# Kernel tuning notes

Hardware: AMD Instinct MI355X
Metric: run time of the kernel (lower is better)

Reference implementation:

```python
import jax, jax.numpy as jnp
import numpy as np

D_MODEL = 512
STATE_DIM = 64
INNER = 768  # ceil(512 * 1.5)
KERNEL = 3
EPS = 1e-5
DELTA_MIN = 1e-4
DELTA_MAX = 3.0


def _hippo_legS(n):
    A = np.zeros((n, n), dtype=np.float32)
    for i in range(n):
        ci = np.sqrt(2 * i + 1)
        for m in range(i + 1):
            cm = np.sqrt(2 * m + 1)
            if i == m:
                A[i, m] = -(2 * i + 1)
            else:
                sign = -1.0 if (i - m) % 2 == 0 else 1.0
                A[i, m] = sign * ci * cm
    idx = np.arange(n, dtype=np.float32)
    B = np.sqrt(2.0 * idx + 1.0)
    C = B.copy()
    C[1::2] *= -1.0
    return A, B, C


def setup_inputs() -> dict:
    key = jax.random.key(0)
    k1, k2, k3, k4 = jax.random.split(key, 4)
    x = jax.random.normal(k1, (8, 2048, D_MODEL), dtype=jnp.float32)
    norm_w = jnp.ones((D_MODEL,), jnp.float32)
    norm_b = jnp.zeros((D_MODEL,), jnp.float32)
    W_in = jax.random.normal(k2, (D_MODEL, 3 * INNER), jnp.float32) * 0.02
    conv_w = jax.random.normal(k3, (INNER, KERNEL), jnp.float32) * 0.2  # torch (C,1,k) squeezed
    A_np, B_np, C_np = _hippo_legS(STATE_DIM)
    scale = 1.0 / np.sqrt(INNER)
    A = jnp.asarray(A_np)
    B_mat = jnp.asarray(np.repeat(B_np[:, None], INNER, axis=1) * scale)   # [N, inner]
    C_mat = jnp.asarray(np.repeat(C_np[None, :], INNER, axis=0) * scale)   # [inner, N]
    W_out = jax.random.normal(k4, (INNER, D_MODEL), jnp.float32) * 0.02
    return {"x": x, "norm_w": norm_w, "norm_b": norm_b, "W_in": W_in,
            "conv_w": conv_w, "A": A, "B_mat": B_mat, "C_mat": C_mat, "W_out": W_out}


def reference(x, norm_w, norm_b, W_in, conv_w, A, B_mat, C_mat, W_out):
    Bsz, L, D = x.shape
    N = A.shape[0]
    # LayerNorm (biased variance, as torch)
    mu = x.mean(-1, keepdims=True)
    var = jnp.mean((x - mu) ** 2, axis=-1, keepdims=True)
    h = (x - mu) / jnp.sqrt(var + EPS) * norm_w + norm_b
    proj = h @ W_in                                 # [B, L, 3*inner]
    data, gate, delta_raw = jnp.split(proj, 3, axis=-1)
    # causal depthwise conv: torch pads k-1 both sides then truncates to L
    k = conv_w.shape[1]
    xp = jnp.pad(data, ((0, 0), (k - 1, 0), (0, 0)))
    kern = conv_w.T[:, None, :]                     # [k, 1, inner] (WIO)
    conv = jax.lax.conv_general_dilated(
        xp, kern, window_strides=(1,), padding='VALID',
        dimension_numbers=('NWC', 'WIO', 'NWC'), feature_group_count=INNER)
    u = jax.nn.silu(conv)                           # [B, L, inner]
    delta = jnp.minimum(jax.nn.softplus(delta_raw).mean(-1) + DELTA_MIN, DELTA_MAX)  # [B, L]
    I = jnp.eye(N, dtype=x.dtype)

    def step(state, inp):
        u_t, dt = inp                               # [B, inner], [B]
        Bu = jnp.einsum('nd,bd->bn', B_mat, u_t)    # [B, N]
        rhs = state + dt[:, None] * Bu
        mat = I - dt[:, None, None] * A             # [B, N, N]
        st = jnp.linalg.solve(mat, rhs[..., None])[..., 0]
        y = jnp.einsum('dn,bn->bd', C_mat, st)      # [B, inner]
        return st, y

    state0 = jnp.zeros((Bsz, N), x.dtype)
    _, ys = jax.lax.scan(step, state0, (jnp.swapaxes(u, 0, 1), delta.T))
    selective = jnp.swapaxes(ys, 0, 1)              # [B, L, inner]
    gated = jax.nn.sigmoid(gate) * selective
    return x + gated @ W_out
```

## Files before the change

### kernel.cpp

```cpp
#include <hip/hip_runtime.h>

typedef unsigned short u16;
typedef short short8 __attribute__((ext_vector_type(8)));
typedef float f32x4 __attribute__((ext_vector_type(4)));

#define D_MODEL 512
#define INNER 768
#define N3 2304
#define LSEQ 2048
#define BATCH 8
#define MROWS 16384

constexpr size_t OFF_H     = 0;
constexpr size_t OFF_WINT  = 16777216;
constexpr size_t OFF_WOUTT = 19136512;
constexpr size_t OFF_DATA  = 19922944;
constexpr size_t OFF_GATE  = 45088768;
constexpr size_t OFF_DSUM  = 70254592;
constexpr size_t OFF_YBAR  = 70451200;
constexpr size_t WS_NEEDED = 70516736;

__device__ __forceinline__ u16 f2bf(float f) {
  unsigned u = __builtin_bit_cast(unsigned, f);
  u += 0x7fffu + ((u >> 16) & 1u);
  return (u16)(u >> 16);
}
__device__ __forceinline__ float bf2f(u16 h) {
  unsigned u = ((unsigned)h) << 16;
  return __builtin_bit_cast(float, u);
}

__device__ __forceinline__ float dpp_shr1(float x) {
  int r = __builtin_amdgcn_update_dpp(0, __builtin_bit_cast(int, x),
                                      0x138 , 0xf, 0xf, true);
  return __builtin_bit_cast(float, r);
}

#if __has_builtin(__builtin_amdgcn_global_load_lds)
#define HAVE_GLLDS 1
__device__ __forceinline__ void gl_lds16(const u16* g, u16* l) {
  __builtin_amdgcn_global_load_lds(
      (const __attribute__((address_space(1))) unsigned int*)g,
      (__attribute__((address_space(3))) unsigned int*)l, 16, 0, 0);
}
#else
#define HAVE_GLLDS 0
#endif

__global__ __launch_bounds__(256) void transp_cast(const float* __restrict__ in,
                                                   u16* __restrict__ out, int R, int C) {
  __shared__ float tile[32][33];
  int c0 = blockIdx.x * 32, r0 = blockIdx.y * 32;
  int tx = threadIdx.x, ty = threadIdx.y;
#pragma unroll
  for (int i = 0; i < 4; ++i)
    tile[ty + i * 8][tx] = in[(size_t)(r0 + ty + i * 8) * C + c0 + tx];
  __syncthreads();
#pragma unroll
  for (int i = 0; i < 4; ++i)
    out[(size_t)(c0 + ty + i * 8) * R + r0 + tx] = f2bf(tile[tx][ty + i * 8]);
}

__global__ __launch_bounds__(256) void ln_kernel(const float* __restrict__ x,
                                                 const float* __restrict__ gw,
                                                 const float* __restrict__ gb,
                                                 u16* __restrict__ h) {
  int row = blockIdx.x * 4 + (threadIdx.x >> 6);
  int lane = threadIdx.x & 63;
  const float* xr = x + (size_t)row * D_MODEL;
  float4 v0 = *(const float4*)(xr + lane * 4);
  float4 v1 = *(const float4*)(xr + 256 + lane * 4);
  float s  = v0.x + v0.y + v0.z + v0.w + v1.x + v1.y + v1.z + v1.w;
  float s2 = v0.x * v0.x + v0.y * v0.y + v0.z * v0.z + v0.w * v0.w +
             v1.x * v1.x + v1.y * v1.y + v1.z * v1.z + v1.w * v1.w;
#pragma unroll
  for (int m = 1; m < 64; m <<= 1) { s += __shfl_xor(s, m); s2 += __shfl_xor(s2, m); }
  float mu = s * (1.0f / 512.0f);
  float var = s2 * (1.0f / 512.0f) - mu * mu;
  float rstd = rsqrtf(var + 1e-5f);
  float4 w0 = *(const float4*)(gw + lane * 4);
  float4 w1 = *(const float4*)(gw + 256 + lane * 4);
  float4 b0 = *(const float4*)(gb + lane * 4);
  float4 b1 = *(const float4*)(gb + 256 + lane * 4);
  float y0 = (v0.x - mu) * rstd * w0.x + b0.x;
  float y1 = (v0.y - mu) * rstd * w0.y + b0.y;
  float y2 = (v0.z - mu) * rstd * w0.z + b0.z;
  float y3 = (v0.w - mu) * rstd * w0.w + b0.w;
  float y4 = (v1.x - mu) * rstd * w1.x + b1.x;
  float y5 = (v1.y - mu) * rstd * w1.y + b1.y;
  float y6 = (v1.z - mu) * rstd * w1.z + b1.z;
  float y7 = (v1.w - mu) * rstd * w1.w + b1.w;
  uint2 pa, pb;
  pa.x = (unsigned)f2bf(y0) | ((unsigned)f2bf(y1) << 16);
  pa.y = (unsigned)f2bf(y2) | ((unsigned)f2bf(y3) << 16);
  pb.x = (unsigned)f2bf(y4) | ((unsigned)f2bf(y5) << 16);
  pb.y = (unsigned)f2bf(y6) | ((unsigned)f2bf(y7) << 16);
  *(uint2*)(h + (size_t)row * D_MODEL + lane * 4) = pa;
  *(uint2*)(h + (size_t)row * D_MODEL + 256 + lane * 4) = pb;
}

template <int MODE>
__global__ __launch_bounds__(256) void gemm_bt(
    const u16* __restrict__ A, const u16* __restrict__ BT, int M, int N, int K,
    u16* __restrict__ dataBuf, u16* __restrict__ gateSig, float* __restrict__ deltaSum,
    const float* __restrict__ ybarp, const float* __restrict__ xres,
    float* __restrict__ outp) {
  __shared__ u16 As[128 * 32];
  __shared__ u16 Bs[128 * 32];
  int tid = threadIdx.x;
  int lane = tid & 63, wv = tid >> 6;
  int wm = wv >> 1, wn = wv & 1;
  int m0 = blockIdx.y * 128, n0 = blockIdx.x * 128;
  f32x4 acc[4][4];
#pragma unroll
  for (int i = 0; i < 4; ++i)
#pragma unroll
    for (int j = 0; j < 4; ++j) acc[i][j] = (f32x4)0.0f;

  int r4 = tid >> 2;
  int c4 = (tid & 3) * 8;
  int nsteps = K >> 5;
  int mrow = wm * 64 + (lane & 15);
  int nrow = wn * 64 + (lane & 15);
  int kq = (lane >> 4) * 8;

  const u16* Ab = A + (size_t)(m0 + r4) * K + c4;
  const u16* Bb = BT + (size_t)(n0 + r4) * K + c4;
  const size_t rowA = (size_t)64 * K, rowB = (size_t)64 * K;
  u16* lA0 = &As[tid * 8];
  u16* lA1 = &As[(tid + 256) * 8];
  u16* lB0 = &Bs[tid * 8];
  u16* lB1 = &Bs[(tid + 256) * 8];

  for (int step = 0; step < nsteps; ++step) {
    int k0 = step * 32;
    __syncthreads();
#if HAVE_GLLDS
    gl_lds16(Ab + k0, lA0);
    gl_lds16(Ab + k0 + rowA, lA1);
    gl_lds16(Bb + k0, lB0);
    gl_lds16(Bb + k0 + rowB, lB1);
#else
    uint4 a0 = *(const uint4*)(Ab + k0);
    uint4 a1 = *(const uint4*)(Ab + k0 + rowA);
    uint4 b0 = *(const uint4*)(Bb + k0);
    uint4 b1 = *(const uint4*)(Bb + k0 + rowB);
    *(uint4*)lA0 = a0; *(uint4*)lA1 = a1;
    *(uint4*)lB0 = b0; *(uint4*)lB1 = b1;
#endif
    __syncthreads();
    short8 af[4], bfr[4];
#pragma unroll
    for (int mt = 0; mt < 4; ++mt)
      af[mt] = *(const short8*)(&As[(mrow + mt * 16) * 32 + kq]);
#pragma unroll
    for (int nt = 0; nt < 4; ++nt)
      bfr[nt] = *(const short8*)(&Bs[(nrow + nt * 16) * 32 + kq]);
#pragma unroll
    for (int mt = 0; mt < 4; ++mt)
#pragma unroll
      for (int nt = 0; nt < 4; ++nt)
        acc[mt][nt] = __builtin_amdgcn_mfma_f32_16x16x32_bf16(af[mt], bfr[nt], acc[mt][nt], 0, 0, 0);
  }

  if (MODE == 1) {
    int region = (n0 >= 1536) ? 2 : (n0 >= 768 ? 1 : 0);
    if (region < 2) {
      u16* dst = (region == 0) ? dataBuf : gateSig;
#pragma unroll
      for (int mt = 0; mt < 4; ++mt) {
        int rbase = m0 + wm * 64 + mt * 16 + (lane >> 4) * 4;
#pragma unroll
        for (int nt = 0; nt < 4; ++nt) {
          int col = n0 - region * 768 + wn * 64 + nt * 16 + (lane & 15);
#pragma unroll
          for (int r = 0; r < 4; ++r) {
            float val = acc[mt][nt][r];
            if (region == 1) val = 1.0f / (1.0f + __expf(-val));
            dst[(size_t)(rbase + r) * INNER + col] = f2bf(val);
          }
        }
      }
    } else {
#pragma unroll
      for (int mt = 0; mt < 4; ++mt) {
        int rbase = m0 + wm * 64 + mt * 16 + (lane >> 4) * 4;
        float sums[4] = {0.f, 0.f, 0.f, 0.f};
#pragma unroll
        for (int nt = 0; nt < 4; ++nt)
#pragma unroll
          for (int r = 0; r < 4; ++r) {
            float xv = acc[mt][nt][r];
            sums[r] += fmaxf(xv, 0.0f) + __logf(1.0f + __expf(-fabsf(xv)));
          }
#pragma unroll
        for (int r = 0; r < 4; ++r) {
          float val = sums[r];
          val += __shfl_xor(val, 1); val += __shfl_xor(val, 2);
          val += __shfl_xor(val, 4); val += __shfl_xor(val, 8);
          if ((lane & 15) == 0) atomicAdd(&deltaSum[rbase + r], val);
        }
      }
    }
  } else {
#pragma unroll
    for (int mt = 0; mt < 4; ++mt) {
      int rbase = m0 + wm * 64 + mt * 16 + (lane >> 4) * 4;
#pragma unroll
      for (int r = 0; r < 4; ++r) {
        float yr = ybarp[rbase + r] * 0.036084391824351615f;
#pragma unroll
        for (int nt = 0; nt < 4; ++nt) {
          int col = n0 + wn * 64 + nt * 16 + (lane & 15);
          size_t o = (size_t)(rbase + r) * D_MODEL + col;
          outp[o] = xres[o] + yr * acc[mt][nt][r];
        }
      }
    }
  }
}

__global__ __launch_bounds__(256) void conv_reduce(const u16* __restrict__ dataBuf,
                                                   const float* __restrict__ conv_w,
                                                   const float* __restrict__ deltaSum,
                                                   float2* __restrict__ pairsG) {
  int r = blockIdx.x;
  int b = r >> 11;
  int t = r & (LSEQ - 1);
  int tid = threadIdx.x;
  float part = 0.0f;
#pragma unroll
  for (int j = 0; j < 3; ++j) {
    int d = tid + j * 256;
    float cw0 = conv_w[d * 3 + 0], cw1 = conv_w[d * 3 + 1], cw2 = conv_w[d * 3 + 2];
    float x2 = bf2f(dataBuf[(size_t)r * INNER + d]);
    float x1 = (t >= 1) ? bf2f(dataBuf[(size_t)(r - 1) * INNER + d]) : 0.0f;
    float x0 = (t >= 2) ? bf2f(dataBuf[(size_t)(r - 2) * INNER + d]) : 0.0f;
    float c = cw0 * x0 + cw1 * x1 + cw2 * x2;
    part += c / (1.0f + __expf(-c));
  }
#pragma unroll
  for (int m = 1; m < 64; m <<= 1) part += __shfl_xor(part, m);
  __shared__ float red[4];
  if ((tid & 63) == 0) red[tid >> 6] = part;
  __syncthreads();
  if (tid == 0) {
    float tot = red[0] + red[1] + red[2] + red[3];
    float v = 0.036084391824351615f * tot;
    float dt = fminf(deltaSum[r] * (1.0f / 768.0f) + 1e-4f, 3.0f);
    pairsG[b * 2240 + 64 + t] = make_float2(dt, dt * v);
  }
  if (tid == 64 && t < 64)   pairsG[b * 2240 + t] = make_float2(0.f, 0.f);
  if (tid == 128 && t < 128) pairsG[b * 2240 + 2112 + t] = make_float2(0.f, 0.f);
}

__global__ __launch_bounds__(64) void ssm_scan(const float2* __restrict__ pairsG,
                                               float* __restrict__ ybar) {
  const int b = blockIdx.x;
  const int lane = threadIdx.x;
  const float2* pb = pairsG + b * 2240 + 64 - lane;
  float* yb = ybar + b * LSEQ;

  const float ddi = 2.0f * lane + 1.0f;
  const float ci = sqrtf(ddi);
  const float di = (lane & 1) ? -ci : ci;

  float2 buf[64];
#pragma unroll
  for (int j = 0; j < 32; ++j) buf[j] = pb[j];

  float P = 0.0f;
  float R = buf[0].y * ci;

  for (int blk = 0; blk < 33; ++blk) {
    int colli = 0;
    const float2* pl = pb + blk * 64 + 32;
#pragma unroll
    for (int u = 0; u < 64; ++u) {
      const int s1 = (u + 1) & 63;
      const int sl = (u + 32) & 63;
      float dt = buf[u].x;
      float gn = buf[s1].y * ci;
      float denom = fmaf(dt, ddi, 1.0f);
      float rr = __builtin_amdgcn_rcpf(denom);
      float rdi = rr * di;
      float rdiR = rdi * R;
      float dtdi = dt * di;
      float Pin = dpp_shr1(P);
      P = fmaf(rr, Pin, rdiR);
      float t1 = fmaf(-dtdi, Pin, R);
      R = fmaf(rr, t1, gn);
      int pv = __builtin_amdgcn_readlane(__builtin_bit_cast(int, P), 63);
      colli = (lane == u) ? pv : colli;
      buf[sl] = pl[u];
    }
    int t_store = blk * 64 - 63 + lane;
    if ((unsigned)t_store < (unsigned)LSEQ)
      yb[t_store] = __builtin_bit_cast(float, colli);
  }
}

extern "C" void kernel_launch(void* const* d_in, const int* in_sizes, int n_in,
                              void* d_out, int out_size, void* d_ws, size_t ws_size,
                              hipStream_t stream) {
  const float* x      = (const float*)d_in[0];
  const float* norm_w = (const float*)d_in[1];
  const float* norm_b = (const float*)d_in[2];
  const float* W_in   = (const float*)d_in[3];
  const float* conv_w = (const float*)d_in[4];
  const float* W_out  = (const float*)d_in[8];
  float* out = (float*)d_out;
  if (ws_size < WS_NEEDED) return;

  char* ws = (char*)d_ws;
  u16* h        = (u16*)(ws + OFF_H);
  u16* WinT     = (u16*)(ws + OFF_WINT);
  u16* WoutT    = (u16*)(ws + OFF_WOUTT);
  u16* dataBuf  = (u16*)(ws + OFF_DATA);
  u16* gateSig  = (u16*)(ws + OFF_GATE);
  float* dSum   = (float*)(ws + OFF_DSUM);
  float* ybar   = (float*)(ws + OFF_YBAR);
  float2* pairsG = (float2*)(ws + OFF_H);

  (void)hipMemsetAsync(dSum, 0, MROWS * sizeof(float), stream);
  transp_cast<<<dim3(N3 / 32, D_MODEL / 32), dim3(32, 8), 0, stream>>>(W_in, WinT, D_MODEL, N3);
  transp_cast<<<dim3(D_MODEL / 32, INNER / 32), dim3(32, 8), 0, stream>>>(W_out, WoutT, INNER, D_MODEL);
  ln_kernel<<<MROWS / 4, 256, 0, stream>>>(x, norm_w, norm_b, h);
  gemm_bt<1><<<dim3(N3 / 128, MROWS / 128), 256, 0, stream>>>(
      h, WinT, MROWS, N3, D_MODEL, dataBuf, gateSig, dSum, nullptr, nullptr, nullptr);
  conv_reduce<<<MROWS, 256, 0, stream>>>(dataBuf, conv_w, dSum, pairsG);
  ssm_scan<<<BATCH, 64, 0, stream>>>(pairsG, ybar);
  gemm_bt<2><<<dim3(D_MODEL / 128, MROWS / 128), 256, 0, stream>>>(
      gateSig, WoutT, MROWS, D_MODEL, INNER, nullptr, nullptr, nullptr, ybar, x, out);
}
```

Before: 299.9 us.

## Load GEMM fragments directly from global memory and remap blocks per XCD

Both projection GEMMs stop staging tiles through LDS and stop using barriers. Each lane now loads its MFMA operand fragments straight from global memory with compile-time K and a 2x unrolled loop. The grid becomes 1D and is remapped so each XCD owns a contiguous band of row tiles, which should improve L2 reuse of A rows. The trade-off is that loads are no longer shared: data the block previously staged once is fetched per wave, increasing global/L2 traffic and possibly exposing latency.

```diff
diff --git a/kernel.cpp b/kernel.cpp
--- a/kernel.cpp
+++ b/kernel.cpp
@@ -35,17 +35,6 @@
                                       0x138 , 0xf, 0xf, true);
   return __builtin_bit_cast(float, r);
 }
-
-#if __has_builtin(__builtin_amdgcn_global_load_lds)
-#define HAVE_GLLDS 1
-__device__ __forceinline__ void gl_lds16(const u16* g, u16* l) {
-  __builtin_amdgcn_global_load_lds(
-      (const __attribute__((address_space(1))) unsigned int*)g,
-      (__attribute__((address_space(3))) unsigned int*)l, 16, 0, 0);
-}
-#else
-#define HAVE_GLLDS 0
-#endif
 
 __global__ __launch_bounds__(256) void transp_cast(const float* __restrict__ in,
                                                    u16* __restrict__ out, int R, int C) {
@@ -99,63 +88,47 @@
   *(uint2*)(h + (size_t)row * D_MODEL + 256 + lane * 4) = pb;
 }
 
-template <int MODE>
-__global__ __launch_bounds__(256) void gemm_bt(
-    const u16* __restrict__ A, const u16* __restrict__ BT, int M, int N, int K,
+template <int MODE, int KK>
+__global__ __launch_bounds__(256) void gemm_direct(
+    const u16* __restrict__ A, const u16* __restrict__ BT,
     u16* __restrict__ dataBuf, u16* __restrict__ gateSig, float* __restrict__ deltaSum,
     const float* __restrict__ ybarp, const float* __restrict__ xres,
     float* __restrict__ outp) {
-  __shared__ u16 As[128 * 32];
-  __shared__ u16 Bs[128 * 32];
+  constexpr int XT = (MODE == 1) ? 18 : 4;
+  int bi = blockIdx.x;
+  int xcd = bi & 7, s = bi >> 3;
+  int ytile = xcd * 16 + s / XT;
+  int xtile = s % XT;
+  int m0 = ytile * 128, n0 = xtile * 128;
+
   int tid = threadIdx.x;
   int lane = tid & 63, wv = tid >> 6;
   int wm = wv >> 1, wn = wv & 1;
-  int m0 = blockIdx.y * 128, n0 = blockIdx.x * 128;
+
   f32x4 acc[4][4];
 #pragma unroll
   for (int i = 0; i < 4; ++i)
 #pragma unroll
     for (int j = 0; j < 4; ++j) acc[i][j] = (f32x4)0.0f;
 
-  int r4 = tid >> 2;
-  int c4 = (tid & 3) * 8;
-  int nsteps = K >> 5;
-  int mrow = wm * 64 + (lane & 15);
-  int nrow = wn * 64 + (lane & 15);
-  int kq = (lane >> 4) * 8;
-
-  const u16* Ab = A + (size_t)(m0 + r4) * K + c4;
-  const u16* Bb = BT + (size_t)(n0 + r4) * K + c4;
-  const size_t rowA = (size_t)64 * K, rowB = (size_t)64 * K;
-  u16* lA0 = &As[tid * 8];
-  u16* lA1 = &As[(tid + 256) * 8];
-  u16* lB0 = &Bs[tid * 8];
-  u16* lB1 = &Bs[(tid + 256) * 8];
-
-  for (int step = 0; step < nsteps; ++step) {
+  const u16* Abase[4];
+  const u16* Bbase[4];
+#pragma unroll
+  for (int mt = 0; mt < 4; ++mt)
+    Abase[mt] = A + (size_t)(m0 + wm * 64 + mt * 16 + (lane & 15)) * KK + (lane >> 4) * 8;
+#pragma unroll
+  for (int nt = 0; nt < 4; ++nt)
+    Bbase[nt] = BT + (size_t)(n0 + wn * 64 + nt * 16 + (lane & 15)) * KK + (lane >> 4) * 8;
+
+  constexpr int NSTEP = KK / 32;
+#pragma unroll 2
+  for (int step = 0; step < NSTEP; ++step) {
     int k0 = step * 32;
-    __syncthreads();
-#if HAVE_GLLDS
-    gl_lds16(Ab + k0, lA0);
-    gl_lds16(Ab + k0 + rowA, lA1);
-    gl_lds16(Bb + k0, lB0);
-    gl_lds16(Bb + k0 + rowB, lB1);
-#else
-    uint4 a0 = *(const uint4*)(Ab + k0);
-    uint4 a1 = *(const uint4*)(Ab + k0 + rowA);
-    uint4 b0 = *(const uint4*)(Bb + k0);
-    uint4 b1 = *(const uint4*)(Bb + k0 + rowB);
-    *(uint4*)lA0 = a0; *(uint4*)lA1 = a1;
-    *(uint4*)lB0 = b0; *(uint4*)lB1 = b1;
-#endif
-    __syncthreads();
     short8 af[4], bfr[4];
 #pragma unroll
-    for (int mt = 0; mt < 4; ++mt)
-      af[mt] = *(const short8*)(&As[(mrow + mt * 16) * 32 + kq]);
-#pragma unroll
-    for (int nt = 0; nt < 4; ++nt)
-      bfr[nt] = *(const short8*)(&Bs[(nrow + nt * 16) * 32 + kq]);
+    for (int mt = 0; mt < 4; ++mt) af[mt] = *(const short8*)(Abase[mt] + k0);
+#pragma unroll
+    for (int nt = 0; nt < 4; ++nt) bfr[nt] = *(const short8*)(Bbase[nt] + k0);
 #pragma unroll
     for (int mt = 0; mt < 4; ++mt)
 #pragma unroll
@@ -326,10 +299,10 @@
   transp_cast<<<dim3(N3 / 32, D_MODEL / 32), dim3(32, 8), 0, stream>>>(W_in, WinT, D_MODEL, N3);
   transp_cast<<<dim3(D_MODEL / 32, INNER / 32), dim3(32, 8), 0, stream>>>(W_out, WoutT, INNER, D_MODEL);
   ln_kernel<<<MROWS / 4, 256, 0, stream>>>(x, norm_w, norm_b, h);
-  gemm_bt<1><<<dim3(N3 / 128, MROWS / 128), 256, 0, stream>>>(
-      h, WinT, MROWS, N3, D_MODEL, dataBuf, gateSig, dSum, nullptr, nullptr, nullptr);
+  gemm_direct<1, 512><<<18 * 128, 256, 0, stream>>>(
+      h, WinT, dataBuf, gateSig, dSum, nullptr, nullptr, nullptr);
   conv_reduce<<<MROWS, 256, 0, stream>>>(dataBuf, conv_w, dSum, pairsG);
   ssm_scan<<<BATCH, 64, 0, stream>>>(pairsG, ybar);
-  gemm_bt<2><<<dim3(D_MODEL / 128, MROWS / 128), 256, 0, stream>>>(
-      gateSig, WoutT, MROWS, D_MODEL, INNER, nullptr, nullptr, nullptr, ybar, x, out);
-}
+  gemm_direct<2, 768><<<4 * 128, 256, 0, stream>>>(
+      gateSig, WoutT, nullptr, nullptr, nullptr, ybar, x, out);
+}
```

New measurement: 412.5 us. 37.5% more time.
